# Kernel tuning notes

Hardware: AMD Instinct MI355X
Metric: run time of the kernel (lower is better)

Reference implementation:

```python
import jax, jax.numpy as jnp
import numpy as np

N = 1048576   # points
C = 50000     # clusters
F1, F2, FO = 128, 64, 64

def _lin(k, out_d, in_d):
    w = jax.random.normal(k, (out_d, in_d), jnp.float32) * (1.0 / np.sqrt(in_d))
    return w

def setup_inputs() -> dict:
    key = jax.random.key(0)
    ks = jax.random.split(key, 13)
    points = jax.random.normal(ks[0], (N, 3), jnp.float32)
    inv_feats = jax.random.normal(ks[1], (N, 4), jnp.float32)
    cluster = jax.random.randint(ks[2], (N,), 0, C, dtype=jnp.int32)
    return {
        "points": points, "inv_feats": inv_feats, "cluster": cluster,
        "W1": _lin(ks[3], F2, 4),       "b1": jnp.zeros((F2,), jnp.float32),
        "W2": _lin(ks[4], F1, F2),      "b2": jnp.zeros((F1,), jnp.float32),
        "W3": _lin(ks[5], F2, F1),      "b3": jnp.zeros((F2,), jnp.float32),
        "W4": _lin(ks[6], FO, F2),      "b4": jnp.zeros((FO,), jnp.float32),
        "W5": _lin(ks[7], 3, FO + 3),   "b5": jnp.zeros((3,), jnp.float32),
    }

def reference(points, inv_feats, cluster, W1, b1, W2, b2, W3, b3, W4, b4, W5, b5):
    relu = jax.nn.relu
    fc1 = relu(inv_feats @ W1.T + b1)                 # [N, F2]
    fc2 = relu(fc1 @ W2.T + b2)                       # [N, F1]
    # global_max_pool over clusters; fc2 >= 0 so clamping empty segments (-inf) to 0 is safe
    mx = jax.ops.segment_max(fc2, cluster, num_segments=C)
    mx = jnp.maximum(mx, 0.0)                         # [C, F1]
    fc3 = relu(mx @ W3.T + b3)                        # [C, F2]
    fc4 = relu(fc3 @ W4.T + b4)                       # [C, FO]
    repeated = fc4[cluster]                           # gather [N, FO]
    concat = jnp.concatenate([points, repeated], axis=-1)  # [N, FO+3]
    fc5 = relu(concat @ W5.T + b5)                    # [N, 3]
    sums = jax.ops.segment_sum(fc5, cluster, num_segments=C)
    cnt = jax.ops.segment_sum(jnp.ones((fc5.shape[0], 1), fc5.dtype), cluster, num_segments=C)
    angles = jax.nn.sigmoid(sums / jnp.maximum(cnt, 1.0))  # [C, 3]
    return (fc4, angles)
```

## Files before the change

### kernel.cpp

```cpp
#include <hip/hip_runtime.h>

#define N_PTS 1048576
#define NC 50000
#define SCAN_B 196

typedef int   i32x4  __attribute__((ext_vector_type(4)));
typedef float f32x4v __attribute__((ext_vector_type(4)));

__device__ __forceinline__ unsigned short bf16rne(float f) {
    unsigned u = __float_as_uint(f);
    u = (u + 0x7fffu + ((u >> 16) & 1u)) >> 16;
    return (unsigned short)u;
}
__device__ __forceinline__ f32x4v mfma16(i32x4 a, i32x4 b, f32x4v c) {
    asm("v_mfma_f32_16x16x32_bf16 %0, %1, %2, %0" : "+v"(c) : "v"(a), "v"(b));
    return c;
}
__device__ __forceinline__ int cvtpk(float lo, float hi) {
    int r;
    asm("v_cvt_pk_bf16_f32 %0, %1, %2" : "=v"(r) : "v"(lo), "v"(hi));
    return r;
}

#define DPPSHR(D, X) __builtin_amdgcn_update_dpp(0, (X), 0x110 | (D), 0xf, 0xf, true)
#define DPPSHL1(X)   __builtin_amdgcn_update_dpp(0, (X), 0x101, 0xf, 0xf, true)

__global__ __launch_bounds__(256) void k_prep(
    const float* __restrict__ W2, const float* __restrict__ W3,
    const float* __restrict__ W4,
    unsigned short* __restrict__ W2bf, unsigned short* __restrict__ W3bf,
    unsigned short* __restrict__ W4bf)
{
    int i = blockIdx.x * 256 + threadIdx.x;
    if (i < 8192)       W2bf[i]         = bf16rne(W2[i]);
    else if (i < 16384) W3bf[i - 8192]  = bf16rne(W3[i - 8192]);
    else                W4bf[i - 16384] = bf16rne(W4[i - 16384]);
}

__global__ __launch_bounds__(256) void k_hist(
    const int* __restrict__ cluster, int* __restrict__ counts)
{
    int i = blockIdx.x * 256 + threadIdx.x;
    atomicAdd(counts + cluster[i], 1);
}

__device__ __forceinline__ int block_excl_scan256(int v, int* lsum, int tid) {
    const int lane = tid & 63, wv = tid >> 6;
    int x = v, u;
    u = __shfl_up(x, 1, 64);  if (lane >= 1)  x += u;
    u = __shfl_up(x, 2, 64);  if (lane >= 2)  x += u;
    u = __shfl_up(x, 4, 64);  if (lane >= 4)  x += u;
    u = __shfl_up(x, 8, 64);  if (lane >= 8)  x += u;
    u = __shfl_up(x, 16, 64); if (lane >= 16) x += u;
    u = __shfl_up(x, 32, 64); if (lane >= 32) x += u;
    if (lane == 63) lsum[wv] = x;
    __syncthreads();
    int woff = 0;
    if (wv > 0) woff += lsum[0];
    if (wv > 1) woff += lsum[1];
    if (wv > 2) woff += lsum[2];
    return woff + x - v;
}

__global__ __launch_bounds__(256) void k_scanA(
    const int* __restrict__ counts, int* __restrict__ partial)
{
    __shared__ int lsum[4];
    int i = blockIdx.x * 256 + threadIdx.x;
    int v = (i < NC) ? counts[i] : 0;
    int e = block_excl_scan256(v, lsum, threadIdx.x);
    if (threadIdx.x == 255) partial[blockIdx.x] = e + v;
}

__global__ __launch_bounds__(256) void k_scanB(int* __restrict__ partial)
{
    __shared__ int lsum[4];
    int tid = threadIdx.x;
    int v = (tid < SCAN_B) ? partial[tid] : 0;
    int e = block_excl_scan256(v, lsum, tid);
    __syncthreads();
    if (tid < SCAN_B) partial[tid] = e;
}

__global__ __launch_bounds__(256) void k_scanC(
    const int* __restrict__ counts, const int* __restrict__ partial,
    int* __restrict__ cursor)
{
    __shared__ int lsum[4];
    int i = blockIdx.x * 256 + threadIdx.x;
    int v = (i < NC) ? counts[i] : 0;
    int e = block_excl_scan256(v, lsum, threadIdx.x);
    if (i < NC) cursor[i] = partial[blockIdx.x] + e;
}

__global__ __launch_bounds__(256) void k_scatter(
    const int* __restrict__ cluster, int* __restrict__ cursor,
    int* __restrict__ perm, int* __restrict__ pclus)
{
    int i = blockIdx.x * 256 + threadIdx.x;
    int c = cluster[i];
    int pos = atomicAdd(cursor + c, 1);
    perm[pos] = i;
    pclus[pos] = c;
}

__global__ __launch_bounds__(256, 4) void k_points_mfma(
    const float* __restrict__ inv_feats,
    const int* __restrict__ perm, const int* __restrict__ pclus,
    const float* __restrict__ W1, const float* __restrict__ b1,
    const unsigned short* __restrict__ W2bf, const float* __restrict__ b2,
    int bofs, float* __restrict__ mx)
{
    const int tid  = threadIdx.x;
    const int wv   = tid >> 6;
    const int l    = tid & 63;
    const int base = (((bofs + blockIdx.x) * 4 + wv)) * 32;
    const int m16 = l & 15;
    const int g4  = (l >> 4) * 4;
    const int k8  = (l >> 4) * 8;

    const int pA = perm[base + m16];
    const int pB = perm[base + 16 + m16];
    const float4 xA = *(const float4*)(inv_feats + (size_t)pA * 4);
    const float4 xB = *(const float4*)(inv_feats + (size_t)pB * 4);

#define ROW2(K, QA, QB) float QA, QB; { \
    const float4 w = *(const float4*)(W1 + (size_t)(K) * 4); \
    const float bb = b1[K]; \
    float a = bb; \
    a = fmaf(w.x, xA.x, a); a = fmaf(w.y, xA.y, a); \
    a = fmaf(w.z, xA.z, a); a = fmaf(w.w, xA.w, a); \
    QA = fmaxf(a, 0.f); \
    float b = bb; \
    b = fmaf(w.x, xB.x, b); b = fmaf(w.y, xB.y, b); \
    b = fmaf(w.z, xB.z, b); b = fmaf(w.w, xB.w, b); \
    QB = fmaxf(b, 0.f); }

    i32x4 b00, b01, b10, b11;
    {
        ROW2(k8 + 0, qa0, qb0) ROW2(k8 + 1, qa1, qb1)
        ROW2(k8 + 2, qa2, qb2) ROW2(k8 + 3, qa3, qb3)
        ROW2(k8 + 4, qa4, qb4) ROW2(k8 + 5, qa5, qb5)
        ROW2(k8 + 6, qa6, qb6) ROW2(k8 + 7, qa7, qb7)
        b00[0] = cvtpk(qa0, qa1); b00[1] = cvtpk(qa2, qa3);
        b00[2] = cvtpk(qa4, qa5); b00[3] = cvtpk(qa6, qa7);
        b10[0] = cvtpk(qb0, qb1); b10[1] = cvtpk(qb2, qb3);
        b10[2] = cvtpk(qb4, qb5); b10[3] = cvtpk(qb6, qb7);
    }
    {
        ROW2(32 + k8 + 0, qa0, qb0) ROW2(32 + k8 + 1, qa1, qb1)
        ROW2(32 + k8 + 2, qa2, qb2) ROW2(32 + k8 + 3, qa3, qb3)
        ROW2(32 + k8 + 4, qa4, qb4) ROW2(32 + k8 + 5, qa5, qb5)
        ROW2(32 + k8 + 6, qa6, qb6) ROW2(32 + k8 + 7, qa7, qb7)
        b01[0] = cvtpk(qa0, qa1); b01[1] = cvtpk(qa2, qa3);
        b01[2] = cvtpk(qa4, qa5); b01[3] = cvtpk(qa6, qa7);
        b11[0] = cvtpk(qb0, qb1); b11[1] = cvtpk(qb2, qb3);
        b11[2] = cvtpk(qb4, qb5); b11[3] = cvtpk(qb6, qb7);
    }
#undef ROW2

    const int cp0 = pclus[base + m16] + 1;
    const int cp1 = pclus[base + 16 + m16] + 1;
    const bool e0a = (DPPSHR(1, cp0) == cp0);
    const bool e0b = (DPPSHR(2, cp0) == cp0);
    const bool e0c = (DPPSHR(4, cp0) == cp0);
    const bool e0d = (DPPSHR(8, cp0) == cp0);
    const bool tl0 = (DPPSHL1(cp0) != cp0);
    const bool e1a = (DPPSHR(1, cp1) == cp1);
    const bool e1b = (DPPSHR(2, cp1) == cp1);
    const bool e1c = (DPPSHR(4, cp1) == cp1);
    const bool e1d = (DPPSHR(8, cp1) == cp1);
    const bool tl1 = (DPPSHL1(cp1) != cp1);
    int* mrow0 = (int*)mx + (size_t)(cp0 - 1) * 128;
    int* mrow1 = (int*)mx + (size_t)(cp1 - 1) * 128;

#define LDA(MB, KK) (*(const i32x4*)(W2bf + (size_t)(kcc + (MB)*16 + m16) * 64 + (KK)*32 + k8))

#define SC4(V, EA, EB, EC, ED) { float _u; \
    _u = __int_as_float(DPPSHR(1, __float_as_int(V))); if (EA) V = fmaxf(V, _u); \
    _u = __int_as_float(DPPSHR(2, __float_as_int(V))); if (EB) V = fmaxf(V, _u); \
    _u = __int_as_float(DPPSHR(4, __float_as_int(V))); if (EC) V = fmaxf(V, _u); \
    _u = __int_as_float(DPPSHR(8, __float_as_int(V))); if (ED) V = fmaxf(V, _u); }

#define EMIT(ACC, MB, EA, EB, EC, ED, TL, MROW) { \
    const float4 bb = *(const float4*)(b2 + kcc + (MB)*16 + g4); \
    float v0 = fmaxf(ACC[0] + bb.x, 0.f); \
    float v1 = fmaxf(ACC[1] + bb.y, 0.f); \
    float v2 = fmaxf(ACC[2] + bb.z, 0.f); \
    float v3 = fmaxf(ACC[3] + bb.w, 0.f); \
    SC4(v0, EA, EB, EC, ED) SC4(v1, EA, EB, EC, ED) \
    SC4(v2, EA, EB, EC, ED) SC4(v3, EA, EB, EC, ED) \
    if (TL) { \
        if (v0 > 0.f) atomicMax(MROW + kcc + (MB)*16 + g4 + 0, __float_as_int(v0)); \
        if (v1 > 0.f) atomicMax(MROW + kcc + (MB)*16 + g4 + 1, __float_as_int(v1)); \
        if (v2 > 0.f) atomicMax(MROW + kcc + (MB)*16 + g4 + 2, __float_as_int(v2)); \
        if (v3 > 0.f) atomicMax(MROW + kcc + (MB)*16 + g4 + 3, __float_as_int(v3)); } }

#define PASS(KC) { \
    const int kcc = (KC) * 64; \
    const i32x4 a00 = LDA(0,0), a01 = LDA(0,1), a10 = LDA(1,0), a11 = LDA(1,1); \
    const i32x4 a20 = LDA(2,0), a21 = LDA(2,1), a30 = LDA(3,0), a31 = LDA(3,1); \
    f32x4v c00 = {0.f,0.f,0.f,0.f}, c01 = {0.f,0.f,0.f,0.f}; \
    f32x4v c10 = {0.f,0.f,0.f,0.f}, c11 = {0.f,0.f,0.f,0.f}; \
    f32x4v c20 = {0.f,0.f,0.f,0.f}, c21 = {0.f,0.f,0.f,0.f}; \
    f32x4v c30 = {0.f,0.f,0.f,0.f}, c31 = {0.f,0.f,0.f,0.f}; \
    c00 = mfma16(a00, b00, c00); c00 = mfma16(a01, b01, c00); \
    c10 = mfma16(a10, b00, c10); c10 = mfma16(a11, b01, c10); \
    c20 = mfma16(a20, b00, c20); c20 = mfma16(a21, b01, c20); \
    c30 = mfma16(a30, b00, c30); c30 = mfma16(a31, b01, c30); \
    c01 = mfma16(a00, b10, c01); c01 = mfma16(a01, b11, c01); \
    c11 = mfma16(a10, b10, c11); c11 = mfma16(a11, b11, c11); \
    c21 = mfma16(a20, b10, c21); c21 = mfma16(a21, b11, c21); \
    c31 = mfma16(a30, b10, c31); c31 = mfma16(a31, b11, c31); \
    EMIT(c00, 0, e0a, e0b, e0c, e0d, tl0, mrow0) \
    EMIT(c10, 1, e0a, e0b, e0c, e0d, tl0, mrow0) \
    EMIT(c20, 2, e0a, e0b, e0c, e0d, tl0, mrow0) \
    EMIT(c30, 3, e0a, e0b, e0c, e0d, tl0, mrow0) \
    EMIT(c01, 0, e1a, e1b, e1c, e1d, tl1, mrow1) \
    EMIT(c11, 1, e1a, e1b, e1c, e1d, tl1, mrow1) \
    EMIT(c21, 2, e1a, e1b, e1c, e1d, tl1, mrow1) \
    EMIT(c31, 3, e1a, e1b, e1c, e1d, tl1, mrow1) }

    PASS(0)
    PASS(1)
#undef PASS
#undef EMIT
#undef SC4
#undef LDA
}

__global__ __launch_bounds__(256, 4) void k_cluster_mfma(
    const float* __restrict__ mx,
    const unsigned short* __restrict__ W3bf, const float* __restrict__ b3,
    const unsigned short* __restrict__ W4bf, const float* __restrict__ b4,
    float* __restrict__ fc4out)
{
    __shared__ __align__(16) unsigned short f3[4][32 * 64];
    const int tid = threadIdx.x;
    const int wv  = tid >> 6;
    const int l   = tid & 63;
    const int m16 = l & 15;
    const int g4  = (l >> 4) * 4;
    const int k8  = (l >> 4) * 8;
    const int cbase = (blockIdx.x * 4 + wv) * 32;
    const int cA = cbase + m16;
    const int cB = cbase + 16 + m16;
    const size_t rA = (size_t)min(cA, NC - 1) * 128;
    const size_t rB = (size_t)min(cB, NC - 1) * 128;
    unsigned short* f3w = &f3[wv][0];
    const int swA = (m16 & 7) << 3;
    const int swB = swA;

    f32x4v d00 = {0,0,0,0}, d01 = {0,0,0,0}, d02 = {0,0,0,0}, d03 = {0,0,0,0};
    f32x4v d10 = {0,0,0,0}, d11 = {0,0,0,0}, d12 = {0,0,0,0}, d13 = {0,0,0,0};

#define LD3(MB, KK) (*(const i32x4*)(W3bf + (size_t)((MB)*16 + m16) * 128 + (KK)*32 + k8))
#define FC3STEP(KK) { \
    const float4 vA0 = *(const float4*)(mx + rA + (KK)*32 + k8); \
    const float4 vA1 = *(const float4*)(mx + rA + (KK)*32 + k8 + 4); \
    const float4 vB0 = *(const float4*)(mx + rB + (KK)*32 + k8); \
    const float4 vB1 = *(const float4*)(mx + rB + (KK)*32 + k8 + 4); \
    i32x4 bA = { cvtpk(vA0.x, vA0.y), cvtpk(vA0.z, vA0.w), \
                 cvtpk(vA1.x, vA1.y), cvtpk(vA1.z, vA1.w) }; \
    i32x4 bB = { cvtpk(vB0.x, vB0.y), cvtpk(vB0.z, vB0.w), \
                 cvtpk(vB1.x, vB1.y), cvtpk(vB1.z, vB1.w) }; \
    const i32x4 a0 = LD3(0, KK), a1 = LD3(1, KK), a2 = LD3(2, KK), a3 = LD3(3, KK); \
    d00 = mfma16(a0, bA, d00); d01 = mfma16(a1, bA, d01); \
    d02 = mfma16(a2, bA, d02); d03 = mfma16(a3, bA, d03); \
    d10 = mfma16(a0, bB, d10); d11 = mfma16(a1, bB, d11); \
    d12 = mfma16(a2, bB, d12); d13 = mfma16(a3, bB, d13); }
    FC3STEP(0) FC3STEP(1) FC3STEP(2) FC3STEP(3)
#undef FC3STEP
#undef LD3

#define ST3(DD, MB, CL, SW) { \
    const float4 bb = *(const float4*)(b3 + (MB)*16 + g4); \
    float v0 = fmaxf(DD[0] + bb.x, 0.f); \
    float v1 = fmaxf(DD[1] + bb.y, 0.f); \
    float v2 = fmaxf(DD[2] + bb.z, 0.f); \
    float v3 = fmaxf(DD[3] + bb.w, 0.f); \
    int2 pk = { cvtpk(v0, v1), cvtpk(v2, v3) }; \
    *(int2*)(f3w + (CL)*64 + ((((MB)*16 + g4)) ^ (SW))) = pk; }
    ST3(d00, 0, m16, swA) ST3(d01, 1, m16, swA) ST3(d02, 2, m16, swA) ST3(d03, 3, m16, swA)
    ST3(d10, 0, 16 + m16, swB) ST3(d11, 1, 16 + m16, swB) ST3(d12, 2, 16 + m16, swB) ST3(d13, 3, 16 + m16, swB)
#undef ST3

    f32x4v e00 = {0,0,0,0}, e01 = {0,0,0,0}, e02 = {0,0,0,0}, e03 = {0,0,0,0};
    f32x4v e10 = {0,0,0,0}, e11 = {0,0,0,0}, e12 = {0,0,0,0}, e13 = {0,0,0,0};
#define LD4(MB, KK) (*(const i32x4*)(W4bf + (size_t)((MB)*16 + m16) * 64 + (KK)*32 + k8))
#define FC4STEP(KK) { \
    const i32x4 bA4 = *(const i32x4*)(f3w + m16*64 + (((KK)*32 + k8) ^ swA)); \
    const i32x4 bB4 = *(const i32x4*)(f3w + (16 + m16)*64 + (((KK)*32 + k8) ^ swB)); \
    const i32x4 a0 = LD4(0, KK), a1 = LD4(1, KK), a2 = LD4(2, KK), a3 = LD4(3, KK); \
    e00 = mfma16(a0, bA4, e00); e01 = mfma16(a1, bA4, e01); \
    e02 = mfma16(a2, bA4, e02); e03 = mfma16(a3, bA4, e03); \
    e10 = mfma16(a0, bB4, e10); e11 = mfma16(a1, bB4, e11); \
    e12 = mfma16(a2, bB4, e12); e13 = mfma16(a3, bB4, e13); }
    FC4STEP(0) FC4STEP(1)
#undef FC4STEP
#undef LD4

#define WR(EE, MB, CL) if ((CL) < NC) { \
    const float4 bb = *(const float4*)(b4 + (MB)*16 + g4); \
    float4 o; \
    o.x = fmaxf(EE[0] + bb.x, 0.f); \
    o.y = fmaxf(EE[1] + bb.y, 0.f); \
    o.z = fmaxf(EE[2] + bb.z, 0.f); \
    o.w = fmaxf(EE[3] + bb.w, 0.f); \
    *(float4*)(fc4out + (size_t)(CL)*64 + (MB)*16 + g4) = o; }
    WR(e00, 0, cA) WR(e01, 1, cA) WR(e02, 2, cA) WR(e03, 3, cA)
    WR(e10, 0, cB) WR(e11, 1, cB) WR(e12, 2, cB) WR(e13, 3, cB)
#undef WR
}

__global__ __launch_bounds__(256) void k_fc5_sorted(
    const float* __restrict__ points,
    const int* __restrict__ perm, const int* __restrict__ pclus,
    const float* __restrict__ fc4, const float* __restrict__ W5,
    const float* __restrict__ b5, float* __restrict__ sums)
{
    const int t = blockIdx.x * 256 + threadIdx.x;
    const int p = perm[t];
    const int c = pclus[t];
    const float p0 = points[(size_t)p * 3 + 0];
    const float p1 = points[(size_t)p * 3 + 1];
    const float p2 = points[(size_t)p * 3 + 2];
    const float* f4 = fc4 + (size_t)c * 64;

    float a0 = b5[0];
    a0 = fmaf(W5[0], p0, a0); a0 = fmaf(W5[1], p1, a0); a0 = fmaf(W5[2], p2, a0);
    float a1 = b5[1];
    a1 = fmaf(W5[67], p0, a1); a1 = fmaf(W5[68], p1, a1); a1 = fmaf(W5[69], p2, a1);
    float a2 = b5[2];
    a2 = fmaf(W5[134], p0, a2); a2 = fmaf(W5[135], p1, a2); a2 = fmaf(W5[136], p2, a2);

#pragma unroll
    for (int j = 0; j < 64; j += 4) {
        float4 v = *(const float4*)(f4 + j);
        a0 = fmaf(W5[3 + j + 0], v.x, a0);
        a0 = fmaf(W5[3 + j + 1], v.y, a0);
        a0 = fmaf(W5[3 + j + 2], v.z, a0);
        a0 = fmaf(W5[3 + j + 3], v.w, a0);
        a1 = fmaf(W5[70 + j + 0], v.x, a1);
        a1 = fmaf(W5[70 + j + 1], v.y, a1);
        a1 = fmaf(W5[70 + j + 2], v.z, a1);
        a1 = fmaf(W5[70 + j + 3], v.w, a1);
        a2 = fmaf(W5[137 + j + 0], v.x, a2);
        a2 = fmaf(W5[137 + j + 1], v.y, a2);
        a2 = fmaf(W5[137 + j + 2], v.z, a2);
        a2 = fmaf(W5[137 + j + 3], v.w, a2);
    }
    a0 = fmaxf(a0, 0.f);
    a1 = fmaxf(a1, 0.f);
    a2 = fmaxf(a2, 0.f);

    const int lane = threadIdx.x & 63;
    const int cu1  = __shfl_up(c, 1, 64);
    const int cu2  = __shfl_up(c, 2, 64);
    const int cu4  = __shfl_up(c, 4, 64);
    const int cu8  = __shfl_up(c, 8, 64);
    const int cu16 = __shfl_up(c, 16, 64);
    const int cu32 = __shfl_up(c, 32, 64);
    const int cdn  = __shfl_down(c, 1, 64);
    const bool eq0 = (lane >= 1)  && (cu1  == c);
    const bool eq1 = (lane >= 2)  && (cu2  == c);
    const bool eq2 = (lane >= 4)  && (cu4  == c);
    const bool eq3 = (lane >= 8)  && (cu8  == c);
    const bool eq4 = (lane >= 16) && (cu16 == c);
    const bool eq5 = (lane >= 32) && (cu32 == c);
    const bool tail = (lane == 63) || (cdn != c);

    float u0, u1, u2;
    u0 = __shfl_up(a0, 1, 64);  u1 = __shfl_up(a1, 1, 64);  u2 = __shfl_up(a2, 1, 64);
    if (eq0) { a0 += u0; a1 += u1; a2 += u2; }
    u0 = __shfl_up(a0, 2, 64);  u1 = __shfl_up(a1, 2, 64);  u2 = __shfl_up(a2, 2, 64);
    if (eq1) { a0 += u0; a1 += u1; a2 += u2; }
    u0 = __shfl_up(a0, 4, 64);  u1 = __shfl_up(a1, 4, 64);  u2 = __shfl_up(a2, 4, 64);
    if (eq2) { a0 += u0; a1 += u1; a2 += u2; }
    u0 = __shfl_up(a0, 8, 64);  u1 = __shfl_up(a1, 8, 64);  u2 = __shfl_up(a2, 8, 64);
    if (eq3) { a0 += u0; a1 += u1; a2 += u2; }
    u0 = __shfl_up(a0, 16, 64); u1 = __shfl_up(a1, 16, 64); u2 = __shfl_up(a2, 16, 64);
    if (eq4) { a0 += u0; a1 += u1; a2 += u2; }
    u0 = __shfl_up(a0, 32, 64); u1 = __shfl_up(a1, 32, 64); u2 = __shfl_up(a2, 32, 64);
    if (eq5) { a0 += u0; a1 += u1; a2 += u2; }

    if (tail) {
        float* srow = sums + (size_t)c * 3;
        atomicAdd(srow + 0, a0);
        atomicAdd(srow + 1, a1);
        atomicAdd(srow + 2, a2);
    }
}

__global__ __launch_bounds__(256) void k_angles(
    const float* __restrict__ sums, const int* __restrict__ counts,
    float* __restrict__ angout)
{
    int c = blockIdx.x * 256 + threadIdx.x;
    if (c >= NC) return;
    const float cnt = fmaxf((float)counts[c], 1.f);
#pragma unroll
    for (int r = 0; r < 3; ++r) {
        float s = sums[(size_t)c * 3 + r] / cnt;
        angout[(size_t)c * 3 + r] = 1.f / (1.f + expf(-s));
    }
}

extern "C" void kernel_launch(void* const* d_in, const int* in_sizes, int n_in,
                              void* d_out, int out_size, void* d_ws, size_t ws_size,
                              hipStream_t stream) {
    const float* points  = (const float*)d_in[0];
    const float* inv     = (const float*)d_in[1];
    const int*   cluster = (const int*)d_in[2];
    const float* W1 = (const float*)d_in[3];
    const float* b1 = (const float*)d_in[4];
    const float* W2 = (const float*)d_in[5];
    const float* b2 = (const float*)d_in[6];
    const float* W3 = (const float*)d_in[7];
    const float* b3 = (const float*)d_in[8];
    const float* W4 = (const float*)d_in[9];
    const float* b4 = (const float*)d_in[10];
    const float* W5 = (const float*)d_in[11];
    const float* b5 = (const float*)d_in[12];

    float* out    = (float*)d_out;
    float* fc4out = out;
    float* angout = out + (size_t)NC * 64;

    int*   counts = (int*)d_ws;
    float* sums   = (float*)(counts + NC);
    float* mx     = sums + (size_t)NC * 3;
    int*   cursor = (int*)(mx + (size_t)NC * 128);
    int*   perm   = cursor + NC;
    int*   pclus  = perm + N_PTS;
    unsigned short* W2bf = (unsigned short*)(pclus + N_PTS);
    unsigned short* W3bf = W2bf + 8192;
    unsigned short* W4bf = W3bf + 8192;
    int*   partial = (int*)(W4bf + 4096);

    hipMemsetAsync(d_ws, 0, (size_t)(NC + NC * 3 + NC * 128) * sizeof(float), stream);

    k_prep         <<<80, 256, 0, stream>>>(W2, W3, W4, W2bf, W3bf, W4bf);
    k_hist         <<<N_PTS / 256, 256, 0, stream>>>(cluster, counts);
    k_scanA        <<<SCAN_B, 256, 0, stream>>>(counts, partial);
    k_scanB        <<<1, 256, 0, stream>>>(partial);
    k_scanC        <<<SCAN_B, 256, 0, stream>>>(counts, partial, cursor);
    k_scatter      <<<N_PTS / 256, 256, 0, stream>>>(cluster, cursor, perm, pclus);
    k_points_mfma  <<<4096, 256, 0, stream>>>(inv, perm, pclus, W1, b1, W2bf, b2, 0, mx);
    k_points_mfma  <<<4096, 256, 0, stream>>>(inv, perm, pclus, W1, b1, W2bf, b2, 4096, mx);
    k_cluster_mfma <<<(NC + 127) / 128, 256, 0, stream>>>(mx, W3bf, b3, W4bf, b4, fc4out);
    k_fc5_sorted   <<<N_PTS / 256, 256, 0, stream>>>(points, perm, pclus, fc4out, W5, b5, sums);
    k_angles       <<<(NC + 255) / 256, 256, 0, stream>>>(sums, counts, angout);
}
```

Measured before the change: 338.1 us.

## Scatter point data into sorted order and fuse prep, hist and scan kernels

The scatter kernel now writes inv_feats and padded points directly into cluster-sorted arrays, so the MLP and fc5 kernels read them contiguously instead of gathering through a permutation. The weight-conversion and histogram kernels are merged, the single-block scanB is removed by having each scanC block rescan the partial sums, and the two half-sized points launches become one. This removes several launches and the random gathers, at the cost of extra workspace and a sorted-mode fallback that depends on the workspace size.

```diff
diff --git a/kernel.cpp b/kernel.cpp
--- a/kernel.cpp
+++ b/kernel.cpp
@@ -25,7 +25,8 @@
 #define DPPSHR(D, X) __builtin_amdgcn_update_dpp(0, (X), 0x110 | (D), 0xf, 0xf, true)
 #define DPPSHL1(X)   __builtin_amdgcn_update_dpp(0, (X), 0x101, 0xf, 0xf, true)
 
-__global__ __launch_bounds__(256) void k_prep(
+__global__ __launch_bounds__(256) void k_histprep(
+    const int* __restrict__ cluster, int* __restrict__ counts,
     const float* __restrict__ W2, const float* __restrict__ W3,
     const float* __restrict__ W4,
     unsigned short* __restrict__ W2bf, unsigned short* __restrict__ W3bf,
@@ -34,13 +35,7 @@
     int i = blockIdx.x * 256 + threadIdx.x;
     if (i < 8192)       W2bf[i]         = bf16rne(W2[i]);
     else if (i < 16384) W3bf[i - 8192]  = bf16rne(W3[i - 8192]);
-    else                W4bf[i - 16384] = bf16rne(W4[i - 16384]);
-}
-
-__global__ __launch_bounds__(256) void k_hist(
-    const int* __restrict__ cluster, int* __restrict__ counts)
-{
-    int i = blockIdx.x * 256 + threadIdx.x;
+    else if (i < 20480) W4bf[i - 16384] = bf16rne(W4[i - 16384]);
     atomicAdd(counts + cluster[i], 1);
 }
 
@@ -72,57 +67,73 @@
     if (threadIdx.x == 255) partial[blockIdx.x] = e + v;
 }
 
-__global__ __launch_bounds__(256) void k_scanB(int* __restrict__ partial)
-{
-    __shared__ int lsum[4];
-    int tid = threadIdx.x;
-    int v = (tid < SCAN_B) ? partial[tid] : 0;
-    int e = block_excl_scan256(v, lsum, tid);
-    __syncthreads();
-    if (tid < SCAN_B) partial[tid] = e;
-}
-
 __global__ __launch_bounds__(256) void k_scanC(
     const int* __restrict__ counts, const int* __restrict__ partial,
     int* __restrict__ cursor)
 {
     __shared__ int lsum[4];
-    int i = blockIdx.x * 256 + threadIdx.x;
+    __shared__ int tot;
+    const int tid = threadIdx.x;
+    int pv = (tid < SCAN_B && tid < blockIdx.x) ? partial[tid] : 0;
+    int pe = block_excl_scan256(pv, lsum, tid);
+    if (tid == 255) tot = pe + pv;
+    __syncthreads();
+    const int pref = tot;
+    __syncthreads();
+    int i = blockIdx.x * 256 + tid;
     int v = (i < NC) ? counts[i] : 0;
-    int e = block_excl_scan256(v, lsum, threadIdx.x);
-    if (i < NC) cursor[i] = partial[blockIdx.x] + e;
-}
-
+    int e = block_excl_scan256(v, lsum, tid);
+    if (i < NC) cursor[i] = pref + e;
+}
+
+template<bool SORTED>
 __global__ __launch_bounds__(256) void k_scatter(
-    const int* __restrict__ cluster, int* __restrict__ cursor,
-    int* __restrict__ perm, int* __restrict__ pclus)
+    const int* __restrict__ cluster, const float* __restrict__ inv,
+    const float* __restrict__ points, int* __restrict__ cursor,
+    int* __restrict__ perm, int* __restrict__ pclus,
+    float4* __restrict__ invs, float4* __restrict__ ptsc)
 {
     int i = blockIdx.x * 256 + threadIdx.x;
     int c = cluster[i];
     int pos = atomicAdd(cursor + c, 1);
-    perm[pos] = i;
     pclus[pos] = c;
-}
-
+    if (SORTED) {
+        invs[pos] = *(const float4*)(inv + (size_t)i * 4);
+        float4 pt = { points[(size_t)i * 3 + 0], points[(size_t)i * 3 + 1],
+                      points[(size_t)i * 3 + 2], 0.f };
+        ptsc[pos] = pt;
+    } else {
+        perm[pos] = i;
+    }
+}
+
+template<bool SORTED>
 __global__ __launch_bounds__(256, 4) void k_points_mfma(
     const float* __restrict__ inv_feats,
     const int* __restrict__ perm, const int* __restrict__ pclus,
+    const float4* __restrict__ invs,
     const float* __restrict__ W1, const float* __restrict__ b1,
     const unsigned short* __restrict__ W2bf, const float* __restrict__ b2,
-    int bofs, float* __restrict__ mx)
+    float* __restrict__ mx)
 {
     const int tid  = threadIdx.x;
     const int wv   = tid >> 6;
     const int l    = tid & 63;
-    const int base = (((bofs + blockIdx.x) * 4 + wv)) * 32;
+    const int base = (blockIdx.x * 4 + wv) * 32;
     const int m16 = l & 15;
     const int g4  = (l >> 4) * 4;
     const int k8  = (l >> 4) * 8;
 
-    const int pA = perm[base + m16];
-    const int pB = perm[base + 16 + m16];
-    const float4 xA = *(const float4*)(inv_feats + (size_t)pA * 4);
-    const float4 xB = *(const float4*)(inv_feats + (size_t)pB * 4);
+    float4 xA, xB;
+    if (SORTED) {
+        xA = invs[base + m16];
+        xB = invs[base + 16 + m16];
+    } else {
+        const int pA = perm[base + m16];
+        const int pB = perm[base + 16 + m16];
+        xA = *(const float4*)(inv_feats + (size_t)pA * 4);
+        xB = *(const float4*)(inv_feats + (size_t)pB * 4);
+    }
 
 #define ROW2(K, QA, QB) float QA, QB; { \
     const float4 w = *(const float4*)(W1 + (size_t)(K) * 4); \
@@ -313,18 +324,26 @@
 #undef WR
 }
 
+template<bool SORTED>
 __global__ __launch_bounds__(256) void k_fc5_sorted(
     const float* __restrict__ points,
     const int* __restrict__ perm, const int* __restrict__ pclus,
+    const float4* __restrict__ ptsc,
     const float* __restrict__ fc4, const float* __restrict__ W5,
     const float* __restrict__ b5, float* __restrict__ sums)
 {
     const int t = blockIdx.x * 256 + threadIdx.x;
-    const int p = perm[t];
     const int c = pclus[t];
-    const float p0 = points[(size_t)p * 3 + 0];
-    const float p1 = points[(size_t)p * 3 + 1];
-    const float p2 = points[(size_t)p * 3 + 2];
+    float p0, p1, p2;
+    if (SORTED) {
+        const float4 pt = ptsc[t];
+        p0 = pt.x; p1 = pt.y; p2 = pt.z;
+    } else {
+        const int p = perm[t];
+        p0 = points[(size_t)p * 3 + 0];
+        p1 = points[(size_t)p * 3 + 1];
+        p2 = points[(size_t)p * 3 + 2];
+    }
     const float* f4 = fc4 + (size_t)c * 64;
 
     float a0 = b5[0];
@@ -431,24 +450,34 @@
     float* sums   = (float*)(counts + NC);
     float* mx     = sums + (size_t)NC * 3;
     int*   cursor = (int*)(mx + (size_t)NC * 128);
-    int*   perm   = cursor + NC;
-    int*   pclus  = perm + N_PTS;
+    int*   pclus  = cursor + NC;
     unsigned short* W2bf = (unsigned short*)(pclus + N_PTS);
     unsigned short* W3bf = W2bf + 8192;
     unsigned short* W4bf = W3bf + 8192;
     int*   partial = (int*)(W4bf + 4096);
+    int*   perm    = partial + 256;
+    float4* invs   = (float4*)(perm + N_PTS);
+    float4* ptsc   = invs + N_PTS;
+    const size_t needed_sorted = (size_t)((char*)(ptsc + N_PTS) - (char*)d_ws);
+    const bool sorted_mode = ws_size >= needed_sorted;
 
     hipMemsetAsync(d_ws, 0, (size_t)(NC + NC * 3 + NC * 128) * sizeof(float), stream);
 
-    k_prep         <<<80, 256, 0, stream>>>(W2, W3, W4, W2bf, W3bf, W4bf);
-    k_hist         <<<N_PTS / 256, 256, 0, stream>>>(cluster, counts);
-    k_scanA        <<<SCAN_B, 256, 0, stream>>>(counts, partial);
-    k_scanB        <<<1, 256, 0, stream>>>(partial);
-    k_scanC        <<<SCAN_B, 256, 0, stream>>>(counts, partial, cursor);
-    k_scatter      <<<N_PTS / 256, 256, 0, stream>>>(cluster, cursor, perm, pclus);
-    k_points_mfma  <<<4096, 256, 0, stream>>>(inv, perm, pclus, W1, b1, W2bf, b2, 0, mx);
-    k_points_mfma  <<<4096, 256, 0, stream>>>(inv, perm, pclus, W1, b1, W2bf, b2, 4096, mx);
+    k_histprep <<<N_PTS / 256, 256, 0, stream>>>(cluster, counts, W2, W3, W4, W2bf, W3bf, W4bf);
+    k_scanA    <<<SCAN_B, 256, 0, stream>>>(counts, partial);
+    k_scanC    <<<SCAN_B, 256, 0, stream>>>(counts, partial, cursor);
+    if (sorted_mode) {
+        k_scatter<true>     <<<N_PTS / 256, 256, 0, stream>>>(cluster, inv, points, cursor, perm, pclus, invs, ptsc);
+        k_points_mfma<true> <<<N_PTS / 128, 256, 0, stream>>>(inv, perm, pclus, invs, W1, b1, W2bf, b2, mx);
+    } else {
+        k_scatter<false>    <<<N_PTS / 256, 256, 0, stream>>>(cluster, inv, points, cursor, perm, pclus, invs, ptsc);
+        k_points_mfma<false><<<N_PTS / 128, 256, 0, stream>>>(inv, perm, pclus, invs, W1, b1, W2bf, b2, mx);
+    }
     k_cluster_mfma <<<(NC + 127) / 128, 256, 0, stream>>>(mx, W3bf, b3, W4bf, b4, fc4out);
-    k_fc5_sorted   <<<N_PTS / 256, 256, 0, stream>>>(points, perm, pclus, fc4out, W5, b5, sums);
-    k_angles       <<<(NC + 255) / 256, 256, 0, stream>>>(sums, counts, angout);
-}
+    if (sorted_mode) {
+        k_fc5_sorted<true>  <<<N_PTS / 256, 256, 0, stream>>>(points, perm, pclus, ptsc, fc4out, W5, b5, sums);
+    } else {
+        k_fc5_sorted<false> <<<N_PTS / 256, 256, 0, stream>>>(points, perm, pclus, ptsc, fc4out, W5, b5, sums);
+    }
+    k_angles <<<(NC + 255) / 256, 256, 0, stream>>>(sums, counts, angout);
+}
```

Result: faster. 295.7 us (-12.5%).
